# Performance work log

Hardware: AMD Instinct MI355X
Metric: run time of the kernel (lower is better)

## Reference

```python
import jax, jax.numpy as jnp
import numpy as np

B, N, K, H = 2, 2048, 32, 256
SCALE = 16.0
EPS = 1e-5


def _ln(x, g, b):
    mu = x.mean(-1, keepdims=True)
    v = ((x - mu) ** 2).mean(-1, keepdims=True)
    return (x - mu) / jnp.sqrt(v + EPS) * g + b


def _lin(x, w, b):
    return x @ w.T + b


def setup_inputs() -> dict:
    key = jax.random.key(0)
    ks = jax.random.split(key, 32)

    def w(k, shape, fan_in):
        return jax.random.uniform(k, shape, jnp.float32, -1.0, 1.0) / np.sqrt(fan_in)

    inp = {
        "h_V": jax.random.normal(ks[0], (B, N, H), jnp.float32),
        "h_E": jax.random.normal(ks[1], (B, N, K, H), jnp.float32),
        "E_idx": jax.random.randint(ks[2], (B, N, K), 0, N, jnp.int64 if jax.config.jax_enable_x64 else jnp.int32),
        # node-message MLP
        "W1_w": w(ks[3], (H, 3 * H), 3 * H), "W1_b": w(ks[4], (H,), 3 * H),
        "W2_w": w(ks[5], (H, H), H), "W2_b": w(ks[6], (H,), H),
        "W3_w": w(ks[7], (H, H), H), "W3_b": w(ks[8], (H,), H),
        # edge-message MLP
        "W11_w": w(ks[9], (H, 3 * H), 3 * H), "W11_b": w(ks[10], (H,), 3 * H),
        "W12_w": w(ks[11], (H, H), H), "W12_b": w(ks[12], (H,), H),
        "W13_w": w(ks[13], (H, H), H), "W13_b": w(ks[14], (H,), H),
        # information_mix FFN (H -> 2H -> H)
        "Win_w": w(ks[15], (2 * H, H), H), "Win_b": w(ks[16], (2 * H,), H),
        "Wout_w": w(ks[17], (H, 2 * H), 2 * H), "Wout_b": w(ks[18], (H,), 2 * H),
        # LayerNorms
        "n1_g": jnp.ones((H,), jnp.float32), "n1_b": jnp.zeros((H,), jnp.float32),
        "n2_g": jnp.ones((H,), jnp.float32), "n2_b": jnp.zeros((H,), jnp.float32),
        "n3_g": jnp.ones((H,), jnp.float32), "n3_b": jnp.zeros((H,), jnp.float32),
    }
    return inp


def reference(h_V, h_E, E_idx,
              W1_w, W1_b, W2_w, W2_b, W3_w, W3_b,
              W11_w, W11_b, W12_w, W12_b, W13_w, W13_b,
              Win_w, Win_b, Wout_w, Wout_b,
              n1_g, n1_b, n2_g, n2_b, n3_g, n3_b):
    # gather neighbor node features: [B,N,K,H]
    gather = jax.vmap(lambda hv, idx: hv[idx])

    def message(hv, he, Wa, ba, Wb, bb, Wc, bc):
        h_nodes = gather(hv, E_idx)                                   # [B,N,K,H]
        hv_exp = jnp.broadcast_to(hv[:, :, None, :], h_nodes.shape)   # [B,N,K,H]
        h_EV = jnp.concatenate([hv_exp, he, h_nodes], -1)             # [B,N,K,3H]
        h = jax.nn.gelu(_lin(h_EV, Wa, ba), approximate=False)
        h = jax.nn.gelu(_lin(h, Wb, bb), approximate=False)
        return _lin(h, Wc, bc)                                        # [B,N,K,H]

    # node update (dropout is identity in eval)
    m = message(h_V, h_E, W1_w, W1_b, W2_w, W2_b, W3_w, W3_b)
    h_V = _ln(h_V + m.sum(-2) / SCALE, n1_g, n1_b)
    # information_mix FFN
    dh = _lin(jax.nn.gelu(_lin(h_V, Win_w, Win_b), approximate=False), Wout_w, Wout_b)
    h_V = _ln(h_V + dh, n2_g, n2_b)
    # edge update
    m = message(h_V, h_E, W11_w, W11_b, W12_w, W12_b, W13_w, W13_b)
    h_E = _ln(h_E + m, n3_g, n3_b)
    return (h_V, h_E)
```

## Files before the change

kernel.cpp:

```cpp
#include <hip/hip_runtime.h>


using u16 = unsigned short;
using bf16x8 = __attribute__((ext_vector_type(8))) short;
using f32x4  = __attribute__((ext_vector_type(4))) float;

__device__ __forceinline__ float bf2f(u16 h) {
    union { unsigned u; float f; } v; v.u = (unsigned)h << 16; return v.f;
}
__device__ __forceinline__ u16 f2bf(float f) {
    union { float f; unsigned u; } v; v.f = f;
    unsigned r = v.u + 0x7fffu + ((v.u >> 16) & 1u);
    return (u16)(r >> 16);
}
__device__ __forceinline__ float gelu_f(float x) {
    if (!(x > -10.0f)) return 0.0f;
    return 0.5f * x * (1.0f + erff(x * 0.70710678118654752f));
}
__device__ __forceinline__ u16 scrub16(u16 h) {
    return ((h & 0x7F80u) == 0x7F80u) ? (u16)0 : h;
}
__device__ __forceinline__ float sanef(float x) {
    return (x == x && x < 1e30f && x > -1e30f) ? x : 0.0f;
}

__device__ __forceinline__ int detect_f32(const void* probe) {
    const u16* p = (const u16*)probe;
    int ok = 1;
    #pragma unroll
    for (int i = 0; i < 16; ++i) {
        int e = (p[2 * i] >> 7) & 0xFF;
        ok &= (e >= 100) & (e <= 140);
    }
    return !ok;
}
__device__ __forceinline__ int detect_i64(const void* eidx) {
    const int* p = (const int*)eidx;
    return (p[1] | p[3] | p[5] | p[7]) == 0;
}
__device__ __forceinline__ int loadidx(const void* base, int i, int i64) {
    int v = i64 ? (int)((const long long*)base)[i] : ((const int*)base)[i];
    return v & 2047;
}
__device__ __forceinline__ float loadf(const void* base, size_t i, int f32) {
    return sanef(f32 ? ((const float*)base)[i] : bf2f(((const u16*)base)[i]));
}
__device__ __forceinline__ void storef(void* base, size_t i, int f32, float v) {
    if (f32) ((float*)base)[i] = v; else ((u16*)base)[i] = f2bf(v);
}
__device__ __forceinline__ void stage8(const void* base, size_t idx, int f32, u16* dst) {
    u16 t[8];
    if (f32) {
        const float* p = (const float*)base + idx;
        f32x4 a = *(const f32x4*)p;
        f32x4 b = *(const f32x4*)(p + 4);
        t[0]=f2bf(sanef(a[0])); t[1]=f2bf(sanef(a[1]));
        t[2]=f2bf(sanef(a[2])); t[3]=f2bf(sanef(a[3]));
        t[4]=f2bf(sanef(b[0])); t[5]=f2bf(sanef(b[1]));
        t[6]=f2bf(sanef(b[2])); t[7]=f2bf(sanef(b[3]));
    } else {
        *(uint4*)t = *(const uint4*)((const u16*)base + idx);
        #pragma unroll
        for (int i = 0; i < 8; ++i) t[i] = scrub16(t[i]);
    }
    *(uint4*)dst = *(uint4*)t;
}
__device__ __forceinline__ void stage_w(const void* B, int ldb, size_t boff, int k0,
                                        int f32, u16* sW, int tid) {
    #pragma unroll
    for (int j = 0; j < 4; ++j)
        stage8(B, boff + (size_t)tid * ldb + k0 + j * 8, f32, sW + tid * 40 + j * 8);
}
__device__ __forceinline__ void stage_w_copy(const u16* wsrc, u16* sW, int tid) {
    const uint4* s = (const uint4*)wsrc;
    uint4* d = (uint4*)sW;
    #pragma unroll
    for (int i = 0; i < 5; ++i) d[tid + i * 256] = s[tid + i * 256];
}

__device__ __forceinline__ void mma_tiles(const u16* aBase, int aStride, int aOff,
                                          const u16* sW, int wm, int wn, int l15, int quad,
                                          f32x4 acc[2][8]) {
    bf16x8 a0 = *(const bf16x8*)(aBase + (wm * 32 + l15) * aStride + aOff + quad * 8);
    bf16x8 a1 = *(const bf16x8*)(aBase + (wm * 32 + 16 + l15) * aStride + aOff + quad * 8);
    #pragma unroll
    for (int nb = 0; nb < 8; ++nb) {
        bf16x8 bfr = *(const bf16x8*)(sW + (wn * 128 + nb * 16 + l15) * 40 + quad * 8);
        acc[0][nb] = __builtin_amdgcn_mfma_f32_16x16x32_bf16(a0, bfr, acc[0][nb], 0, 0, 0);
        acc[1][nb] = __builtin_amdgcn_mfma_f32_16x16x32_bf16(a1, bfr, acc[1][nb], 0, 0, 0);
    }
}

__global__ __launch_bounds__(256) void prep_k(
    const void* probe, const void* hV,
    const void* W1, const void* W2, const void* W3,
    const void* Win, const void* Wout,
    const void* W11, const void* W12, const void* W13,
    void* dout, void* wsOpt)
{
    const int f32 = detect_f32(probe);
    char* outEb = (char*)dout + (size_t)1048576 * (f32 ? 4 : 2);
    const size_t eoutB = (size_t)33554432 * (f32 ? 4 : 2);
    u16* mainW = (u16*)(outEb + (14u << 20));
    u16* edgeW = wsOpt ? (u16*)wsOpt
                       : (u16*)(outEb + eoutB - (size_t)40 * 20480);
    u16* hV0   = (u16*)(outEb + (16u << 20));

    const int y  = blockIdx.y;
    const int t0 = blockIdx.x * 256 + threadIdx.x;
    const int stride = gridDim.x * 256;

    if (y < 8) {
        const void* srcs[8] = {W1, W2, W3, Win, Wout, W11, W12, W13};
        const int kd[8] = {768, 256, 256, 256, 512, 768, 256, 256};
        const int ne[8] = {196608, 65536, 65536, 131072, 131072, 196608, 65536, 65536};
        const int sb[8] = {0, 24, 32, 40, 56, 0, 24, 32};
        const void* src = srcs[y];
        u16* dstW = (y >= 5) ? edgeW : mainW;
        const int K = kd[y], n = ne[y], s0 = sb[y];
        for (int i = t0; i < n; i += stride) {
            const int row = i / K;
            const int k   = i - row * K;
            const int slot = s0 + (row >> 8) * (K >> 5) + (k >> 5);
            const u16 v = f32 ? f2bf(sanef(((const float*)src)[i]))
                              : scrub16(((const u16*)src)[i]);
            dstW[(size_t)slot * 10240 + (size_t)(row & 255) * 40 + (k & 31)] = v;
        }
    } else {
        for (int g = t0; g < 131072; g += stride) {
            u16 t[8];
            stage8(hV, (size_t)g * 8, f32, t);
            *(uint4*)(hV0 + (size_t)g * 8) = *(uint4*)t;
        }
    }
}

template<int MODE, int SLOTS>
__global__ __launch_bounds__(256, 2) void msg_fused(
    const void* probe, const void* hVcur, const void* hE, const void* Eidx,
    const void* W1, const void* b1, const void* W2, const void* b2,
    const void* W3, const void* b3, const void* lng, const void* lnb,
    void* dout, const void* wsOpt, int blk0)
{
    __shared__ __align__(16) u16 sT[64 * 264];
    __shared__ __align__(16) u16 sW0[256 * 40];
    __shared__ __align__(16) u16 sW1[256 * 40];
    u16* sA0 = sT;
    u16* sA1 = sT + 2560;

    const int f32 = detect_f32(probe);
    const int i64 = detect_i64(Eidx);
    char* outEb = (char*)dout + (size_t)1048576 * (f32 ? 4 : 2);
    const size_t eoutB = (size_t)33554432 * (f32 ? 4 : 2);
    const u16* wsl = (MODE == 0)
        ? (const u16*)(outEb + (14u << 20))
        : (wsOpt ? (const u16*)wsOpt
                 : (const u16*)(outEb + eoutB - (size_t)40 * 20480));
    const u16* hV0 = (const u16*)(outEb + (16u << 20));

    const int tid  = threadIdx.x;
    const int lane = tid & 63;
    const int wv   = tid >> 6;
    const int wm   = wv & 1;
    const int wn   = wv >> 1;
    const int l15  = lane & 15;
    const int quad = lane >> 4;
    const int m0   = (blockIdx.x + blk0) * 64;

    const int r = tid >> 2, c = tid & 3;
    const int mg_r   = m0 + r;
    const int node_r = mg_r >> 5;
    const int bidx_r = mg_r >> 16;
    const int jn_r   = bidx_r * 2048 + loadidx(Eidx, mg_r, i64);
    const size_t selfOff = (size_t)node_r * 256;
    const size_t eOff    = (size_t)mg_r   * 256;
    const size_t nbrOff  = (size_t)jn_r   * 256;

    int col[8];
    #pragma unroll
    for (int nb = 0; nb < 8; ++nb) col[nb] = wn * 128 + nb * 16 + l15;

    const f32x4 vzero = {0.f, 0.f, 0.f, 0.f};
    f32x4 acc[2][8];
    #pragma unroll
    for (int mb = 0; mb < 2; ++mb)
        #pragma unroll
        for (int nb = 0; nb < 8; ++nb) acc[mb][nb] = vzero;

    auto stageW = [&](int ss, u16* dst) {
        if (SLOTS) stage_w_copy(wsl + (size_t)ss * 10240, dst, tid);
        else if (ss < 24) stage_w(W1, 768, 0, ss * 32, f32, dst, tid);
        else if (ss < 32) stage_w(W2, 256, 0, (ss - 24) * 32, f32, dst, tid);
        else              stage_w(W3, 256, 0, (ss - 32) * 32, f32, dst, tid);
    };
    auto stageA = [&](int ks, u16* dstBuf) {
        u16* d = dstBuf + r * 40 + c * 8;
        if (ks < 8 || ks >= 16) {
            const size_t aoff = ((ks < 8) ? selfOff : nbrOff)
                              + (size_t)(ks & 7) * 32 + (size_t)c * 8;
            if (MODE == 0) *(uint4*)d = *(const uint4*)(hV0 + aoff);
            else           stage8(hVcur, aoff, f32, d);
        } else {
            stage8(hE, eOff + (size_t)(ks & 7) * 32 + (size_t)c * 8, f32, d);
        }
    };

    stageW(0, sW0);
    stageA(0, sA0);
    __syncthreads();

    for (int ss = 0; ss < 24; ++ss) {
        u16* sWc = (ss & 1) ? sW1 : sW0;
        u16* sWn = (ss & 1) ? sW0 : sW1;
        u16* sAc = (ss & 1) ? sA1 : sA0;
        u16* sAn = (ss & 1) ? sA0 : sA1;
        mma_tiles(sAc, 40, 0, sWc, wm, wn, l15, quad, acc);
        stageW(ss + 1, sWn);
        if (ss < 23) stageA(ss + 1, sAn);
        __syncthreads();
    }
    {
        float bv[8];
        #pragma unroll
        for (int nb = 0; nb < 8; ++nb) bv[nb] = loadf(b1, col[nb], f32);
        #pragma unroll
        for (int mb = 0; mb < 2; ++mb)
            #pragma unroll
            for (int rr = 0; rr < 4; ++rr) {
                const int row = wm * 32 + mb * 16 + quad * 4 + rr;
                #pragma unroll
                for (int nb = 0; nb < 8; ++nb)
                    sT[row * 264 + col[nb]] = f2bf(gelu_f(acc[mb][nb][rr] + bv[nb]));
            }
    }
    __syncthreads();

    #pragma unroll
    for (int mb = 0; mb < 2; ++mb)
        #pragma unroll
        for (int nb = 0; nb < 8; ++nb) acc[mb][nb] = vzero;
    for (int ss = 24; ss < 32; ++ss) {
        u16* sWc = (ss & 1) ? sW1 : sW0;
        u16* sWn = (ss & 1) ? sW0 : sW1;
        mma_tiles(sT, 264, (ss - 24) * 32, sWc, wm, wn, l15, quad, acc);
        stageW(ss + 1, sWn);
        __syncthreads();
    }
    {
        float bv[8];
        #pragma unroll
        for (int nb = 0; nb < 8; ++nb) bv[nb] = loadf(b2, col[nb], f32);
        #pragma unroll
        for (int mb = 0; mb < 2; ++mb)
            #pragma unroll
            for (int rr = 0; rr < 4; ++rr) {
                const int row = wm * 32 + mb * 16 + quad * 4 + rr;
                #pragma unroll
                for (int nb = 0; nb < 8; ++nb)
                    sT[row * 264 + col[nb]] = f2bf(gelu_f(acc[mb][nb][rr] + bv[nb]));
            }
    }
    __syncthreads();

    #pragma unroll
    for (int mb = 0; mb < 2; ++mb)
        #pragma unroll
        for (int nb = 0; nb < 8; ++nb) acc[mb][nb] = vzero;
    for (int ss = 32; ss < 40; ++ss) {
        u16* sWc = (ss & 1) ? sW1 : sW0;
        u16* sWn = (ss & 1) ? sW0 : sW1;
        mma_tiles(sT, 264, (ss - 32) * 32, sWc, wm, wn, l15, quad, acc);
        if (ss < 39) stageW(ss + 1, sWn);
        __syncthreads();
    }

    if (MODE == 0) {
        float* Msum = (float*)outEb;
        const int node0 = (m0 >> 5) + wm;
        #pragma unroll
        for (int nb = 0; nb < 8; ++nb) {
            float s = acc[0][nb][0] + acc[0][nb][1] + acc[0][nb][2] + acc[0][nb][3]
                    + acc[1][nb][0] + acc[1][nb][1] + acc[1][nb][2] + acc[1][nb][3];
            s += __shfl_xor(s, 16);
            s += __shfl_xor(s, 32);
            if (quad == 0)
                Msum[(size_t)node0 * 256 + col[nb]] = s + 32.0f * loadf(b3, col[nb], f32);
        }
    } else {
        float* sLN = (float*)sT;
        float b3v[8], gv[8], bv[8];
        #pragma unroll
        for (int nb = 0; nb < 8; ++nb) {
            b3v[nb] = loadf(b3, col[nb], f32);
            gv[nb]  = loadf(lng, col[nb], f32);
            bv[nb]  = loadf(lnb, col[nb], f32);
        }
        #pragma unroll
        for (int mb = 0; mb < 2; ++mb)
            #pragma unroll
            for (int rr = 0; rr < 4; ++rr) {
                const int row = wm * 32 + mb * 16 + quad * 4 + rr;
                const size_t ebase = (size_t)(m0 + row) * 256;
                float ps = 0.f, pq = 0.f;
                #pragma unroll
                for (int nb = 0; nb < 8; ++nb) {
                    float v = acc[mb][nb][rr] + b3v[nb] + loadf(hE, ebase + col[nb], f32);
                    acc[mb][nb][rr] = v;
                    ps += v; pq += v * v;
                }
                ps += __shfl_xor(ps, 1);  pq += __shfl_xor(pq, 1);
                ps += __shfl_xor(ps, 2);  pq += __shfl_xor(pq, 2);
                ps += __shfl_xor(ps, 4);  pq += __shfl_xor(pq, 4);
                ps += __shfl_xor(ps, 8);  pq += __shfl_xor(pq, 8);
                if (l15 == 0) {
                    sLN[(wn * 64 + row) * 2]     = ps;
                    sLN[(wn * 64 + row) * 2 + 1] = pq;
                }
            }
        __syncthreads();
        #pragma unroll
        for (int mb = 0; mb < 2; ++mb)
            #pragma unroll
            for (int rr = 0; rr < 4; ++rr) {
                const int row = wm * 32 + mb * 16 + quad * 4 + rr;
                const float ts = sLN[row * 2]     + sLN[(64 + row) * 2];
                const float tq = sLN[row * 2 + 1] + sLN[(64 + row) * 2 + 1];
                const float mu   = ts * (1.0f / 256.0f);
                const float var  = fmaxf(tq * (1.0f / 256.0f) - mu * mu, 0.0f);
                const float rstd = rsqrtf(var + 1e-5f);
                const size_t obase = (size_t)(m0 + row) * 256;
                #pragma unroll
                for (int nb = 0; nb < 8; ++nb)
                    storef(outEb, obase + col[nb], f32,
                           (acc[mb][nb][rr] - mu) * rstd * gv[nb] + bv[nb]);
            }
    }
}

template<int PHASE>
__global__ __launch_bounds__(256, 2) void gemm_ffn(
    const void* probe, void* dout, const void* bias)
{
    __shared__ __align__(16) u16 sW[256 * 40];
    __shared__ __align__(16) u16 sA[64 * 40];

    const int f32 = detect_f32(probe);
    char* outEb = (char*)dout + (size_t)1048576 * (f32 ? 4 : 2);
    const u16* wsl = (const u16*)(outEb + (14u << 20));
    u16*   hV1  = (u16*)(outEb + (4u << 20));
    u16*   Ubuf = (u16*)(outEb + (6u << 20));
    float* dh   = (float*)(outEb + (10u << 20));

    const int tid  = threadIdx.x;
    const int lane = tid & 63;
    const int wv   = tid >> 6;
    const int wm   = wv & 1;
    const int wn   = wv >> 1;
    const int l15  = lane & 15;
    const int quad = lane >> 4;
    const int m0   = blockIdx.x * 64;
    const int colbase = blockIdx.y * 256;
    const int slotBase = (PHASE == 0) ? (40 + (int)blockIdx.y * 8) : 56;

    const int Kdim = (PHASE == 0) ? 256 : 512;
    const u16* A   = (PHASE == 0) ? hV1 : Ubuf;
    const int lda  = (PHASE == 0) ? 256 : 512;

    int col[8];
    #pragma unroll
    for (int nb = 0; nb < 8; ++nb) col[nb] = wn * 128 + nb * 16 + l15;

    const f32x4 vzero = {0.f, 0.f, 0.f, 0.f};
    f32x4 acc[2][8];
    #pragma unroll
    for (int mb = 0; mb < 2; ++mb)
        #pragma unroll
        for (int nb = 0; nb < 8; ++nb) acc[mb][nb] = vzero;

    const int r = tid >> 2, c = tid & 3;
    for (int ks = 0; ks < (Kdim >> 5); ++ks) {
        const int k0 = ks * 32;
        stage_w_copy(wsl + (size_t)(slotBase + ks) * 10240, sW, tid);
        *(uint4*)(sA + r * 40 + c * 8) =
            *(const uint4*)(A + (size_t)(m0 + r) * lda + k0 + c * 8);
        __syncthreads();
        mma_tiles(sA, 40, 0, sW, wm, wn, l15, quad, acc);
        __syncthreads();
    }

    #pragma unroll
    for (int mb = 0; mb < 2; ++mb)
        #pragma unroll
        for (int rr = 0; rr < 4; ++rr) {
            const int row = m0 + wm * 32 + mb * 16 + quad * 4 + rr;
            #pragma unroll
            for (int nb = 0; nb < 8; ++nb) {
                const int gcol = colbase + col[nb];
                const float v = acc[mb][nb][rr] + loadf(bias, gcol, f32);
                if (PHASE == 0)
                    Ubuf[(size_t)row * 512 + gcol] = f2bf(gelu_f(v));
                else
                    dh[(size_t)row * 256 + gcol] = v;
            }
        }
}

template<int PHASE>
__global__ __launch_bounds__(256) void ln_k(
    const void* probe, void* dout, const void* g, const void* b)
{
    const int f32 = detect_f32(probe);
    char* outEb = (char*)dout + (size_t)1048576 * (f32 ? 4 : 2);
    float* Msum = (float*)outEb;
    u16*   hV1  = (u16*)(outEb + (4u << 20));
    float* dh   = (float*)(outEb + (10u << 20));

    const int lane = threadIdx.x & 63;
    const int wvi  = threadIdx.x >> 6;
    const int row  = blockIdx.x * 4 + wvi;
    const size_t base = (size_t)row * 256 + lane * 4;

    float v[4];
    #pragma unroll
    for (int i = 0; i < 4; ++i) {
        float xb = (PHASE == 0) ? loadf(probe, base + i, f32) : bf2f(hV1[base + i]);
        float xf = (PHASE == 0) ? sanef(Msum[base + i]) * (1.0f / 16.0f)
                                : sanef(dh[base + i]);
        v[i] = xb + xf;
    }
    float s = v[0] + v[1] + v[2] + v[3];
    float q = v[0]*v[0] + v[1]*v[1] + v[2]*v[2] + v[3]*v[3];
    #pragma unroll
    for (int d = 1; d < 64; d <<= 1) { s += __shfl_xor(s, d); q += __shfl_xor(q, d); }
    const float mu   = s * (1.0f / 256.0f);
    const float var  = fmaxf(q * (1.0f / 256.0f) - mu * mu, 0.0f);
    const float rstd = rsqrtf(var + 1e-5f);

    #pragma unroll
    for (int i = 0; i < 4; ++i) {
        const float o = (v[i] - mu) * rstd * loadf(g, lane * 4 + i, f32)
                      + loadf(b, lane * 4 + i, f32);
        if (PHASE == 0) hV1[base + i] = f2bf(o);
        else            storef(dout, base + i, f32, o);
    }
}

extern "C" void kernel_launch(void* const* d_in, const int* in_sizes, int n_in,
                              void* d_out, int out_size, void* d_ws, size_t ws_size,
                              hipStream_t stream)
{
    (void)in_sizes; (void)n_in; (void)out_size;
    const void* probe = d_in[0];
    void* wsOpt = (ws_size >= (size_t)40 * 20480) ? d_ws : nullptr;

    prep_k<<<dim3(128, 9), 256, 0, stream>>>(
        probe, d_in[0],
        d_in[3], d_in[5], d_in[7],
        d_in[15], d_in[17],
        d_in[9], d_in[11], d_in[13],
        d_out, wsOpt);

    msg_fused<0, 1><<<dim3(2048), 256, 0, stream>>>(
        probe, nullptr, d_in[1], d_in[2],
        nullptr, d_in[4], nullptr, d_in[6], nullptr, d_in[8],
        nullptr, nullptr, d_out, nullptr, 0);
    ln_k<0><<<dim3(1024), 256, 0, stream>>>(probe, d_out, d_in[19], d_in[20]);

    gemm_ffn<0><<<dim3(64, 2), 256, 0, stream>>>(probe, d_out, d_in[16]);
    gemm_ffn<1><<<dim3(64, 1), 256, 0, stream>>>(probe, d_out, d_in[18]);
    ln_k<1><<<dim3(1024), 256, 0, stream>>>(probe, d_out, d_in[21], d_in[22]);

    if (wsOpt) {
        msg_fused<1, 1><<<dim3(2048), 256, 0, stream>>>(
            probe, d_out, d_in[1], d_in[2],
            nullptr, d_in[10], nullptr, d_in[12], nullptr, d_in[14],
            d_in[23], d_in[24], d_out, wsOpt, 0);
    } else {
        msg_fused<1, 1><<<dim3(2023), 256, 0, stream>>>(
            probe, d_out, d_in[1], d_in[2],
            nullptr, d_in[10], nullptr, d_in[12], nullptr, d_in[14],
            d_in[23], d_in[24], d_out, nullptr, 0);
        msg_fused<1, 0><<<dim3(25), 256, 0, stream>>>(
            probe, d_out, d_in[1], d_in[2],
            d_in[9], d_in[10], d_in[11], d_in[12], d_in[13], d_in[14],
            d_in[23], d_in[24], d_out, nullptr, 2023);
    }
}
```

Measured before the change: 791.9 us.

## Load MFMA operands directly from global memory, dropping LDS weight staging

Removes the double-buffered LDS staging of weight and activation tiles in the message and FFN kernels. Each wave now loads its A fragments and weight fragments straight from global memory into registers for the MFMA. The padded weight slot layout shrinks from 40 to 32 columns, and occupancy is raised to 3 blocks per CU now that shared memory is freed. This removes the per-step barriers and LDS traffic, but every wave redundantly fetches the weight tiles through cache, so global and L2 load pressure rises and latency is no longer hidden by explicit prefetch.

```diff
diff --git a/kernel.cpp b/kernel.cpp
--- a/kernel.cpp
+++ b/kernel.cpp
@@ -65,29 +65,38 @@
     }
     *(uint4*)dst = *(uint4*)t;
 }
-__device__ __forceinline__ void stage_w(const void* B, int ldb, size_t boff, int k0,
-                                        int f32, u16* sW, int tid) {
-    #pragma unroll
-    for (int j = 0; j < 4; ++j)
-        stage8(B, boff + (size_t)tid * ldb + k0 + j * 8, f32, sW + tid * 40 + j * 8);
-}
-__device__ __forceinline__ void stage_w_copy(const u16* wsrc, u16* sW, int tid) {
-    const uint4* s = (const uint4*)wsrc;
-    uint4* d = (uint4*)sW;
-    #pragma unroll
-    for (int i = 0; i < 5; ++i) d[tid + i * 256] = s[tid + i * 256];
-}
-
-__device__ __forceinline__ void mma_tiles(const u16* aBase, int aStride, int aOff,
-                                          const u16* sW, int wm, int wn, int l15, int quad,
-                                          f32x4 acc[2][8]) {
-    bf16x8 a0 = *(const bf16x8*)(aBase + (wm * 32 + l15) * aStride + aOff + quad * 8);
-    bf16x8 a1 = *(const bf16x8*)(aBase + (wm * 32 + 16 + l15) * aStride + aOff + quad * 8);
+
+__device__ __forceinline__ bf16x8 raw8(const u16* p) { return *(const bf16x8*)p; }
+__device__ __forceinline__ bf16x8 scr8(const u16* p) {
+    bf16x8 r = *(const bf16x8*)p;
+    #pragma unroll
+    for (int i = 0; i < 8; ++i) r[i] = (short)scrub16((u16)r[i]);
+    return r;
+}
+__device__ __forceinline__ bf16x8 cvt8(const float* p) {
+    f32x4 a = *(const f32x4*)p;
+    f32x4 b = *(const f32x4*)(p + 4);
+    bf16x8 r;
+    r[0]=(short)f2bf(sanef(a[0])); r[1]=(short)f2bf(sanef(a[1]));
+    r[2]=(short)f2bf(sanef(a[2])); r[3]=(short)f2bf(sanef(a[3]));
+    r[4]=(short)f2bf(sanef(b[0])); r[5]=(short)f2bf(sanef(b[1]));
+    r[6]=(short)f2bf(sanef(b[2])); r[7]=(short)f2bf(sanef(b[3]));
+    return r;
+}
+
+template<int BM>
+__device__ __forceinline__ void mma_nb(bf16x8 a0, bf16x8 a1, const void* B,
+                                       int koff, int pitch, int wn, int l15,
+                                       f32x4 acc[2][8]) {
     #pragma unroll
     for (int nb = 0; nb < 8; ++nb) {
-        bf16x8 bfr = *(const bf16x8*)(sW + (wn * 128 + nb * 16 + l15) * 40 + quad * 8);
-        acc[0][nb] = __builtin_amdgcn_mfma_f32_16x16x32_bf16(a0, bfr, acc[0][nb], 0, 0, 0);
-        acc[1][nb] = __builtin_amdgcn_mfma_f32_16x16x32_bf16(a1, bfr, acc[1][nb], 0, 0, 0);
+        const int colr = wn * 128 + nb * 16 + l15;
+        bf16x8 b;
+        if (BM == 0)      b = raw8((const u16*)B + (size_t)colr * pitch + koff);
+        else if (BM == 1) b = cvt8((const float*)B + (size_t)colr * pitch + koff);
+        else              b = scr8((const u16*)B + (size_t)colr * pitch + koff);
+        acc[0][nb] = __builtin_amdgcn_mfma_f32_16x16x32_bf16(a0, b, acc[0][nb], 0, 0, 0);
+        acc[1][nb] = __builtin_amdgcn_mfma_f32_16x16x32_bf16(a1, b, acc[1][nb], 0, 0, 0);
     }
 }
 
@@ -103,7 +112,7 @@
     const size_t eoutB = (size_t)33554432 * (f32 ? 4 : 2);
     u16* mainW = (u16*)(outEb + (14u << 20));
     u16* edgeW = wsOpt ? (u16*)wsOpt
-                       : (u16*)(outEb + eoutB - (size_t)40 * 20480);
+                       : (u16*)(outEb + eoutB - (size_t)40 * 16384);
     u16* hV0   = (u16*)(outEb + (16u << 20));
 
     const int y  = blockIdx.y;
@@ -124,7 +133,7 @@
             const int slot = s0 + (row >> 8) * (K >> 5) + (k >> 5);
             const u16 v = f32 ? f2bf(sanef(((const float*)src)[i]))
                               : scrub16(((const u16*)src)[i]);
-            dstW[(size_t)slot * 10240 + (size_t)(row & 255) * 40 + (k & 31)] = v;
+            dstW[(size_t)slot * 8192 + (size_t)(row & 255) * 32 + (k & 31)] = v;
         }
     } else {
         for (int g = t0; g < 131072; g += stride) {
@@ -136,17 +145,13 @@
 }
 
 template<int MODE, int SLOTS>
-__global__ __launch_bounds__(256, 2) void msg_fused(
+__global__ __launch_bounds__(256, 3) void msg_fused(
     const void* probe, const void* hVcur, const void* hE, const void* Eidx,
     const void* W1, const void* b1, const void* W2, const void* b2,
     const void* W3, const void* b3, const void* lng, const void* lnb,
     void* dout, const void* wsOpt, int blk0)
 {
     __shared__ __align__(16) u16 sT[64 * 264];
-    __shared__ __align__(16) u16 sW0[256 * 40];
-    __shared__ __align__(16) u16 sW1[256 * 40];
-    u16* sA0 = sT;
-    u16* sA1 = sT + 2560;
 
     const int f32 = detect_f32(probe);
     const int i64 = detect_i64(Eidx);
@@ -155,7 +160,7 @@
     const u16* wsl = (MODE == 0)
         ? (const u16*)(outEb + (14u << 20))
         : (wsOpt ? (const u16*)wsOpt
-                 : (const u16*)(outEb + eoutB - (size_t)40 * 20480));
+                 : (const u16*)(outEb + eoutB - (size_t)40 * 16384));
     const u16* hV0 = (const u16*)(outEb + (16u << 20));
 
     const int tid  = threadIdx.x;
@@ -166,15 +171,13 @@
     const int l15  = lane & 15;
     const int quad = lane >> 4;
     const int m0   = (blockIdx.x + blk0) * 64;
-
-    const int r = tid >> 2, c = tid & 3;
-    const int mg_r   = m0 + r;
-    const int node_r = mg_r >> 5;
-    const int bidx_r = mg_r >> 16;
-    const int jn_r   = bidx_r * 2048 + loadidx(Eidx, mg_r, i64);
-    const size_t selfOff = (size_t)node_r * 256;
-    const size_t eOff    = (size_t)mg_r   * 256;
-    const size_t nbrOff  = (size_t)jn_r   * 256;
+    const int ko4  = quad * 8;
+
+    const int row0 = wm * 32 + l15, row1 = row0 + 16;
+    const int mg0  = m0 + row0,     mg1  = m0 + row1;
+    const int self0 = mg0 >> 5,     self1 = mg1 >> 5;
+    const int jn0 = (mg0 >> 16) * 2048 + loadidx(Eidx, mg0, i64);
+    const int jn1 = (mg1 >> 16) * 2048 + loadidx(Eidx, mg1, i64);
 
     int col[8];
     #pragma unroll
@@ -187,37 +190,56 @@
         #pragma unroll
         for (int nb = 0; nb < 8; ++nb) acc[mb][nb] = vzero;
 
-    auto stageW = [&](int ss, u16* dst) {
-        if (SLOTS) stage_w_copy(wsl + (size_t)ss * 10240, dst, tid);
-        else if (ss < 24) stage_w(W1, 768, 0, ss * 32, f32, dst, tid);
-        else if (ss < 32) stage_w(W2, 256, 0, (ss - 24) * 32, f32, dst, tid);
-        else              stage_w(W3, 256, 0, (ss - 32) * 32, f32, dst, tid);
-    };
-    auto stageA = [&](int ks, u16* dstBuf) {
-        u16* d = dstBuf + r * 40 + c * 8;
-        if (ks < 8 || ks >= 16) {
-            const size_t aoff = ((ks < 8) ? selfOff : nbrOff)
-                              + (size_t)(ks & 7) * 32 + (size_t)c * 8;
-            if (MODE == 0) *(uint4*)d = *(const uint4*)(hV0 + aoff);
-            else           stage8(hVcur, aoff, f32, d);
+    #pragma unroll 2
+    for (int kk = 0; kk < 8; ++kk) {
+        const int ko = kk * 32 + ko4;
+        bf16x8 a0, a1;
+        if (MODE == 0) {
+            a0 = raw8(hV0 + (size_t)self0 * 256 + ko);
+            a1 = raw8(hV0 + (size_t)self1 * 256 + ko);
+        } else if (f32) {
+            a0 = cvt8((const float*)hVcur + (size_t)self0 * 256 + ko);
+            a1 = cvt8((const float*)hVcur + (size_t)self1 * 256 + ko);
         } else {
-            stage8(hE, eOff + (size_t)(ks & 7) * 32 + (size_t)c * 8, f32, d);
-        }
-    };
-
-    stageW(0, sW0);
-    stageA(0, sA0);
-    __syncthreads();
-
-    for (int ss = 0; ss < 24; ++ss) {
-        u16* sWc = (ss & 1) ? sW1 : sW0;
-        u16* sWn = (ss & 1) ? sW0 : sW1;
-        u16* sAc = (ss & 1) ? sA1 : sA0;
-        u16* sAn = (ss & 1) ? sA0 : sA1;
-        mma_tiles(sAc, 40, 0, sWc, wm, wn, l15, quad, acc);
-        stageW(ss + 1, sWn);
-        if (ss < 23) stageA(ss + 1, sAn);
-        __syncthreads();
+            a0 = raw8((const u16*)hVcur + (size_t)self0 * 256 + ko);
+            a1 = raw8((const u16*)hVcur + (size_t)self1 * 256 + ko);
+        }
+        if (SLOTS)    mma_nb<0>(a0, a1, wsl + (size_t)kk * 8192, ko4, 32, wn, l15, acc);
+        else if (f32) mma_nb<1>(a0, a1, W1, kk * 32 + ko4, 768, wn, l15, acc);
+        else          mma_nb<2>(a0, a1, W1, kk * 32 + ko4, 768, wn, l15, acc);
+    }
+    #pragma unroll 2
+    for (int kk = 0; kk < 8; ++kk) {
+        const int ko = kk * 32 + ko4;
+        bf16x8 a0, a1;
+        if (f32) {
+            a0 = cvt8((const float*)hE + (size_t)mg0 * 256 + ko);
+            a1 = cvt8((const float*)hE + (size_t)mg1 * 256 + ko);
+        } else {
+            a0 = scr8((const u16*)hE + (size_t)mg0 * 256 + ko);
+            a1 = scr8((const u16*)hE + (size_t)mg1 * 256 + ko);
+        }
+        if (SLOTS)    mma_nb<0>(a0, a1, wsl + (size_t)(8 + kk) * 8192, ko4, 32, wn, l15, acc);
+        else if (f32) mma_nb<1>(a0, a1, W1, (8 + kk) * 32 + ko4, 768, wn, l15, acc);
+        else          mma_nb<2>(a0, a1, W1, (8 + kk) * 32 + ko4, 768, wn, l15, acc);
+    }
+    #pragma unroll 2
+    for (int kk = 0; kk < 8; ++kk) {
+        const int ko = kk * 32 + ko4;
+        bf16x8 a0, a1;
+        if (MODE == 0) {
+            a0 = raw8(hV0 + (size_t)jn0 * 256 + ko);
+            a1 = raw8(hV0 + (size_t)jn1 * 256 + ko);
+        } else if (f32) {
+            a0 = cvt8((const float*)hVcur + (size_t)jn0 * 256 + ko);
+            a1 = cvt8((const float*)hVcur + (size_t)jn1 * 256 + ko);
+        } else {
+            a0 = raw8((const u16*)hVcur + (size_t)jn0 * 256 + ko);
+            a1 = raw8((const u16*)hVcur + (size_t)jn1 * 256 + ko);
+        }
+        if (SLOTS)    mma_nb<0>(a0, a1, wsl + (size_t)(16 + kk) * 8192, ko4, 32, wn, l15, acc);
+        else if (f32) mma_nb<1>(a0, a1, W1, (16 + kk) * 32 + ko4, 768, wn, l15, acc);
+        else          mma_nb<2>(a0, a1, W1, (16 + kk) * 32 + ko4, 768, wn, l15, acc);
     }
     {
         float bv[8];
@@ -239,13 +261,16 @@
     for (int mb = 0; mb < 2; ++mb)
         #pragma unroll
         for (int nb = 0; nb < 8; ++nb) acc[mb][nb] = vzero;
-    for (int ss = 24; ss < 32; ++ss) {
-        u16* sWc = (ss & 1) ? sW1 : sW0;
-        u16* sWn = (ss & 1) ? sW0 : sW1;
-        mma_tiles(sT, 264, (ss - 24) * 32, sWc, wm, wn, l15, quad, acc);
-        stageW(ss + 1, sWn);
-        __syncthreads();
-    }
+    #pragma unroll 2
+    for (int kk = 0; kk < 8; ++kk) {
+        const int ko = kk * 32 + ko4;
+        bf16x8 a0 = raw8(sT + row0 * 264 + ko);
+        bf16x8 a1 = raw8(sT + row1 * 264 + ko);
+        if (SLOTS)    mma_nb<0>(a0, a1, wsl + (size_t)(24 + kk) * 8192, ko4, 32, wn, l15, acc);
+        else if (f32) mma_nb<1>(a0, a1, W2, kk * 32 + ko4, 256, wn, l15, acc);
+        else          mma_nb<2>(a0, a1, W2, kk * 32 + ko4, 256, wn, l15, acc);
+    }
+    __syncthreads();
     {
         float bv[8];
         #pragma unroll
@@ -266,12 +291,14 @@
     for (int mb = 0; mb < 2; ++mb)
         #pragma unroll
         for (int nb = 0; nb < 8; ++nb) acc[mb][nb] = vzero;
-    for (int ss = 32; ss < 40; ++ss) {
-        u16* sWc = (ss & 1) ? sW1 : sW0;
-        u16* sWn = (ss & 1) ? sW0 : sW1;
-        mma_tiles(sT, 264, (ss - 32) * 32, sWc, wm, wn, l15, quad, acc);
-        if (ss < 39) stageW(ss + 1, sWn);
-        __syncthreads();
+    #pragma unroll 2
+    for (int kk = 0; kk < 8; ++kk) {
+        const int ko = kk * 32 + ko4;
+        bf16x8 a0 = raw8(sT + row0 * 264 + ko);
+        bf16x8 a1 = raw8(sT + row1 * 264 + ko);
+        if (SLOTS)    mma_nb<0>(a0, a1, wsl + (size_t)(32 + kk) * 8192, ko4, 32, wn, l15, acc);
+        else if (f32) mma_nb<1>(a0, a1, W3, kk * 32 + ko4, 256, wn, l15, acc);
+        else          mma_nb<2>(a0, a1, W3, kk * 32 + ko4, 256, wn, l15, acc);
     }
 
     if (MODE == 0) {
@@ -287,6 +314,7 @@
                 Msum[(size_t)node0 * 256 + col[nb]] = s + 32.0f * loadf(b3, col[nb], f32);
         }
     } else {
+        __syncthreads();
         float* sLN = (float*)sT;
         float b3v[8], gv[8], bv[8];
         #pragma unroll
@@ -341,9 +369,6 @@
 __global__ __launch_bounds__(256, 2) void gemm_ffn(
     const void* probe, void* dout, const void* bias)
 {
-    __shared__ __align__(16) u16 sW[256 * 40];
-    __shared__ __align__(16) u16 sA[64 * 40];
-
     const int f32 = detect_f32(probe);
     char* outEb = (char*)dout + (size_t)1048576 * (f32 ? 4 : 2);
     const u16* wsl = (const u16*)(outEb + (14u << 20));
@@ -361,11 +386,14 @@
     const int m0   = blockIdx.x * 64;
     const int colbase = blockIdx.y * 256;
     const int slotBase = (PHASE == 0) ? (40 + (int)blockIdx.y * 8) : 56;
+    const int ko4  = quad * 8;
 
     const int Kdim = (PHASE == 0) ? 256 : 512;
     const u16* A   = (PHASE == 0) ? hV1 : Ubuf;
     const int lda  = (PHASE == 0) ? 256 : 512;
 
+    const int row0 = wm * 32 + l15, row1 = row0 + 16;
+
     int col[8];
     #pragma unroll
     for (int nb = 0; nb < 8; ++nb) col[nb] = wn * 128 + nb * 16 + l15;
@@ -377,15 +405,12 @@
         #pragma unroll
         for (int nb = 0; nb < 8; ++nb) acc[mb][nb] = vzero;
 
-    const int r = tid >> 2, c = tid & 3;
+    #pragma unroll 2
     for (int ks = 0; ks < (Kdim >> 5); ++ks) {
-        const int k0 = ks * 32;
-        stage_w_copy(wsl + (size_t)(slotBase + ks) * 10240, sW, tid);
-        *(uint4*)(sA + r * 40 + c * 8) =
-            *(const uint4*)(A + (size_t)(m0 + r) * lda + k0 + c * 8);
-        __syncthreads();
-        mma_tiles(sA, 40, 0, sW, wm, wn, l15, quad, acc);
-        __syncthreads();
+        const int ko = ks * 32 + ko4;
+        bf16x8 a0 = raw8(A + (size_t)(m0 + row0) * lda + ko);
+        bf16x8 a1 = raw8(A + (size_t)(m0 + row1) * lda + ko);
+        mma_nb<0>(a0, a1, wsl + (size_t)(slotBase + ks) * 8192, ko4, 32, wn, l15, acc);
     }
 
     #pragma unroll
@@ -451,7 +476,7 @@
 {
     (void)in_sizes; (void)n_in; (void)out_size;
     const void* probe = d_in[0];
-    void* wsOpt = (ws_size >= (size_t)40 * 20480) ? d_ws : nullptr;
+    void* wsOpt = (ws_size >= (size_t)40 * 16384) ? d_ws : nullptr;
 
     prep_k<<<dim3(128, 9), 256, 0, stream>>>(
         probe, d_in[0],
@@ -476,13 +501,13 @@
             nullptr, d_in[10], nullptr, d_in[12], nullptr, d_in[14],
             d_in[23], d_in[24], d_out, wsOpt, 0);
     } else {
-        msg_fused<1, 1><<<dim3(2023), 256, 0, stream>>>(
+        msg_fused<1, 1><<<dim3(2028), 256, 0, stream>>>(
             probe, d_out, d_in[1], d_in[2],
             nullptr, d_in[10], nullptr, d_in[12], nullptr, d_in[14],
             d_in[23], d_in[24], d_out, nullptr, 0);
-        msg_fused<1, 0><<<dim3(25), 256, 0, stream>>>(
+        msg_fused<1, 0><<<dim3(20), 256, 0, stream>>>(
             probe, d_out, d_in[1], d_in[2],
             d_in[9], d_in[10], d_in[11], d_in[12], d_in[13], d_in[14],
-            d_in[23], d_in[24], d_out, nullptr, 2023);
-    }
-}
+            d_in[23], d_in[24], d_out, nullptr, 2028);
+    }
+}
```

Result: slower. 1.184 ms (+49.5%).

## Enlarge message-kernel tiles to 256 rows with 1024-thread blocks, single-buffered

Applied to the files above, without the earlier changes.

The fused message kernel now handles 256 edge rows per block with 16 waves instead of 64 rows with 4 waves. Each staged weight K-slice is therefore reused across four times as many rows, cutting repeated weight traffic from global memory into LDS. In exchange, the double-buffered weight and activation staging is replaced by a single buffer with two barriers per K step, so loads no longer overlap the MFMA work. The larger activation tile also raises LDS use to roughly one block per CU.

```diff
diff --git a/kernel.cpp b/kernel.cpp
--- a/kernel.cpp
+++ b/kernel.cpp
@@ -65,11 +65,16 @@
     }
     *(uint4*)dst = *(uint4*)t;
 }
-__device__ __forceinline__ void stage_w(const void* B, int ldb, size_t boff, int k0,
-                                        int f32, u16* sW, int tid) {
-    #pragma unroll
-    for (int j = 0; j < 4; ++j)
-        stage8(B, boff + (size_t)tid * ldb + k0 + j * 8, f32, sW + tid * 40 + j * 8);
+__device__ __forceinline__ void stage_w2(const void* B, int ldb, int k0,
+                                         int f32, u16* sW, int tid) {
+    const int rr = tid >> 2, cc = tid & 3;
+    stage8(B, (size_t)rr * ldb + k0 + cc * 8, f32, sW + rr * 40 + cc * 8);
+}
+__device__ __forceinline__ void stage_w_copy2(const u16* wsrc, u16* sW, int tid) {
+    const uint4* s = (const uint4*)wsrc;
+    uint4* d = (uint4*)sW;
+    d[tid] = s[tid];
+    if (tid < 256) d[1024 + tid] = s[1024 + tid];
 }
 __device__ __forceinline__ void stage_w_copy(const u16* wsrc, u16* sW, int tid) {
     const uint4* s = (const uint4*)wsrc;
@@ -136,17 +141,15 @@
 }
 
 template<int MODE, int SLOTS>
-__global__ __launch_bounds__(256, 2) void msg_fused(
+__global__ __launch_bounds__(1024, 4) void msg_fused(
     const void* probe, const void* hVcur, const void* hE, const void* Eidx,
     const void* W1, const void* b1, const void* W2, const void* b2,
     const void* W3, const void* b3, const void* lng, const void* lnb,
     void* dout, const void* wsOpt, int blk0)
 {
-    __shared__ __align__(16) u16 sT[64 * 264];
-    __shared__ __align__(16) u16 sW0[256 * 40];
-    __shared__ __align__(16) u16 sW1[256 * 40];
-    u16* sA0 = sT;
-    u16* sA1 = sT + 2560;
+    __shared__ __align__(16) u16 sT[256 * 264];
+    __shared__ __align__(16) u16 sW[256 * 40];
+    u16* sA = sT;
 
     const int f32 = detect_f32(probe);
     const int i64 = detect_i64(Eidx);
@@ -161,11 +164,11 @@
     const int tid  = threadIdx.x;
     const int lane = tid & 63;
     const int wv   = tid >> 6;
-    const int wm   = wv & 1;
-    const int wn   = wv >> 1;
+    const int wm   = wv >> 1;
+    const int wn   = wv & 1;
     const int l15  = lane & 15;
     const int quad = lane >> 4;
-    const int m0   = (blockIdx.x + blk0) * 64;
+    const int m0   = (blockIdx.x + blk0) * 256;
 
     const int r = tid >> 2, c = tid & 3;
     const int mg_r   = m0 + r;
@@ -187,14 +190,8 @@
         #pragma unroll
         for (int nb = 0; nb < 8; ++nb) acc[mb][nb] = vzero;
 
-    auto stageW = [&](int ss, u16* dst) {
-        if (SLOTS) stage_w_copy(wsl + (size_t)ss * 10240, dst, tid);
-        else if (ss < 24) stage_w(W1, 768, 0, ss * 32, f32, dst, tid);
-        else if (ss < 32) stage_w(W2, 256, 0, (ss - 24) * 32, f32, dst, tid);
-        else              stage_w(W3, 256, 0, (ss - 32) * 32, f32, dst, tid);
-    };
-    auto stageA = [&](int ks, u16* dstBuf) {
-        u16* d = dstBuf + r * 40 + c * 8;
+    auto stageA = [&](int ks) {
+        u16* d = sA + r * 40 + c * 8;
         if (ks < 8 || ks >= 16) {
             const size_t aoff = ((ks < 8) ? selfOff : nbrOff)
                               + (size_t)(ks & 7) * 32 + (size_t)c * 8;
@@ -205,18 +202,12 @@
         }
     };
 
-    stageW(0, sW0);
-    stageA(0, sA0);
-    __syncthreads();
-
-    for (int ss = 0; ss < 24; ++ss) {
-        u16* sWc = (ss & 1) ? sW1 : sW0;
-        u16* sWn = (ss & 1) ? sW0 : sW1;
-        u16* sAc = (ss & 1) ? sA1 : sA0;
-        u16* sAn = (ss & 1) ? sA0 : sA1;
-        mma_tiles(sAc, 40, 0, sWc, wm, wn, l15, quad, acc);
-        stageW(ss + 1, sWn);
-        if (ss < 23) stageA(ss + 1, sAn);
+    for (int ks = 0; ks < 24; ++ks) {
+        if (SLOTS) stage_w_copy2(wsl + (size_t)ks * 10240, sW, tid);
+        else       stage_w2(W1, 768, ks * 32, f32, sW, tid);
+        stageA(ks);
+        __syncthreads();
+        mma_tiles(sA, 40, 0, sW, wm, wn, l15, quad, acc);
         __syncthreads();
     }
     {
@@ -239,11 +230,11 @@
     for (int mb = 0; mb < 2; ++mb)
         #pragma unroll
         for (int nb = 0; nb < 8; ++nb) acc[mb][nb] = vzero;
-    for (int ss = 24; ss < 32; ++ss) {
-        u16* sWc = (ss & 1) ? sW1 : sW0;
-        u16* sWn = (ss & 1) ? sW0 : sW1;
-        mma_tiles(sT, 264, (ss - 24) * 32, sWc, wm, wn, l15, quad, acc);
-        stageW(ss + 1, sWn);
+    for (int ks = 0; ks < 8; ++ks) {
+        if (SLOTS) stage_w_copy2(wsl + (size_t)(24 + ks) * 10240, sW, tid);
+        else       stage_w2(W2, 256, ks * 32, f32, sW, tid);
+        __syncthreads();
+        mma_tiles(sT, 264, ks * 32, sW, wm, wn, l15, quad, acc);
         __syncthreads();
     }
     {
@@ -266,11 +257,11 @@
     for (int mb = 0; mb < 2; ++mb)
         #pragma unroll
         for (int nb = 0; nb < 8; ++nb) acc[mb][nb] = vzero;
-    for (int ss = 32; ss < 40; ++ss) {
-        u16* sWc = (ss & 1) ? sW1 : sW0;
-        u16* sWn = (ss & 1) ? sW0 : sW1;
-        mma_tiles(sT, 264, (ss - 32) * 32, sWc, wm, wn, l15, quad, acc);
-        if (ss < 39) stageW(ss + 1, sWn);
+    for (int ks = 0; ks < 8; ++ks) {
+        if (SLOTS) stage_w_copy2(wsl + (size_t)(32 + ks) * 10240, sW, tid);
+        else       stage_w2(W3, 256, ks * 32, f32, sW, tid);
+        __syncthreads();
+        mma_tiles(sT, 264, ks * 32, sW, wm, wn, l15, quad, acc);
         __syncthreads();
     }
 
@@ -313,8 +304,8 @@
                 ps += __shfl_xor(ps, 4);  pq += __shfl_xor(pq, 4);
                 ps += __shfl_xor(ps, 8);  pq += __shfl_xor(pq, 8);
                 if (l15 == 0) {
-                    sLN[(wn * 64 + row) * 2]     = ps;
-                    sLN[(wn * 64 + row) * 2 + 1] = pq;
+                    sLN[(wn * 256 + row) * 2]     = ps;
+                    sLN[(wn * 256 + row) * 2 + 1] = pq;
                 }
             }
         __syncthreads();
@@ -323,8 +314,8 @@
             #pragma unroll
             for (int rr = 0; rr < 4; ++rr) {
                 const int row = wm * 32 + mb * 16 + quad * 4 + rr;
-                const float ts = sLN[row * 2]     + sLN[(64 + row) * 2];
-                const float tq = sLN[row * 2 + 1] + sLN[(64 + row) * 2 + 1];
+                const float ts = sLN[row * 2]     + sLN[(256 + row) * 2];
+                const float tq = sLN[row * 2 + 1] + sLN[(256 + row) * 2 + 1];
                 const float mu   = ts * (1.0f / 256.0f);
                 const float var  = fmaxf(tq * (1.0f / 256.0f) - mu * mu, 0.0f);
                 const float rstd = rsqrtf(var + 1e-5f);
@@ -460,7 +451,7 @@
         d_in[9], d_in[11], d_in[13],
         d_out, wsOpt);
 
-    msg_fused<0, 1><<<dim3(2048), 256, 0, stream>>>(
+    msg_fused<0, 1><<<dim3(512), 1024, 0, stream>>>(
         probe, nullptr, d_in[1], d_in[2],
         nullptr, d_in[4], nullptr, d_in[6], nullptr, d_in[8],
         nullptr, nullptr, d_out, nullptr, 0);
@@ -471,18 +462,18 @@
     ln_k<1><<<dim3(1024), 256, 0, stream>>>(probe, d_out, d_in[21], d_in[22]);
 
     if (wsOpt) {
-        msg_fused<1, 1><<<dim3(2048), 256, 0, stream>>>(
+        msg_fused<1, 1><<<dim3(512), 1024, 0, stream>>>(
             probe, d_out, d_in[1], d_in[2],
             nullptr, d_in[10], nullptr, d_in[12], nullptr, d_in[14],
             d_in[23], d_in[24], d_out, wsOpt, 0);
     } else {
-        msg_fused<1, 1><<<dim3(2023), 256, 0, stream>>>(
+        msg_fused<1, 1><<<dim3(505), 1024, 0, stream>>>(
             probe, d_out, d_in[1], d_in[2],
             nullptr, d_in[10], nullptr, d_in[12], nullptr, d_in[14],
             d_in[23], d_in[24], d_out, nullptr, 0);
-        msg_fused<1, 0><<<dim3(25), 256, 0, stream>>>(
+        msg_fused<1, 0><<<dim3(7), 1024, 0, stream>>>(
             probe, d_out, d_in[1], d_in[2],
             d_in[9], d_in[10], d_in[11], d_in[12], d_in[13], d_in[14],
-            d_in[23], d_in[24], d_out, nullptr, 2023);
-    }
-}
+            d_in[23], d_in[24], d_out, nullptr, 505);
+    }
+}
```

Result: faster. 746.2 us (-5.8%).
